# Performance work log

Hardware: AMD Instinct MI355X
Metric: run time of the kernel (lower is better)

The kernel has to match this reference:

```python
import jax, jax.numpy as jnp
import numpy as np

BN_EPS = 1e-5


def _bn_train(x, gamma, beta):
    # BatchNorm1d over channel dim (axis=1) of [B, C, L], training-mode batch stats
    m = jnp.mean(x, axis=(0, 2), keepdims=True)
    v = jnp.var(x, axis=(0, 2), keepdims=True)  # biased, matches torch normalization
    xn = (x - m) * jax.lax.rsqrt(v + BN_EPS)
    return xn * gamma[None, :, None] + beta[None, :, None]


def setup_inputs() -> dict:
    key = jax.random.key(0)
    ks = jax.random.split(key, 9)
    B, d1, d2, dout, p1, p2 = 16, 64, 64, 64, 256, 256
    ini1 = np.sqrt(3.0 / dout / d1)
    ini2 = np.sqrt(3.0 / dout / d2)
    u = lambda k, s, ini: jax.random.uniform(k, s, jnp.float32, -ini, ini)
    return {
        "A_AP": jax.random.normal(ks[0], (B, d1, p1), jnp.float32),
        "A_UE": jax.random.normal(ks[1], (B, d1, p2), jnp.float32),
        "H": jax.random.normal(ks[2], (B, d2, p1, p2), jnp.float32),
        "Q1_AP": u(ks[3], (dout, d1), ini1),
        "Q2_AP": u(ks[4], (dout, d1), ini1),
        "Q1_UE": u(ks[5], (dout, d1), ini1),
        "Q2_UE": u(ks[6], (dout, d1), ini1),
        "P1_AP": u(ks[7], (dout, d2), ini2),
        "P1_UE": u(ks[8], (dout, d2), ini2),
        "gamma": jnp.ones((dout,), jnp.float32),
        "beta": jnp.zeros((dout,), jnp.float32),
        "permutation_size1": p1,
        "permutation_size2": p2,
        "BATCH_SIZE": B,
    }


def reference(A_AP, A_UE, H, Q1_AP, Q2_AP, Q1_UE, Q2_UE, P1_AP, P1_UE,
              gamma, beta, permutation_size1, permutation_size2, BATCH_SIZE):
    # mean-aggregations
    ue_mean = jnp.mean(A_UE, axis=-1)          # [B, d1]
    ap_mean = jnp.mean(A_AP, axis=-1)          # [B, d1]
    h_mean_ue = jnp.mean(H, axis=-1)           # [B, d2, p1]
    h_mean_ap = jnp.mean(H, axis=-2)           # [B, d2, p2]

    ap1 = jnp.einsum('od,bdp->bop', Q1_AP, A_AP)                # [B, out, p1]
    ap2 = jnp.einsum('od,bd->bo', Q2_AP, ue_mean)[:, :, None]   # [B, out, 1]
    ap3 = jnp.einsum('od,bdp->bop', P1_AP, h_mean_ue)           # [B, out, p1]
    ue1 = jnp.einsum('od,bdp->bop', Q1_UE, A_UE)                # [B, out, p2]
    ue2 = jnp.einsum('od,bd->bo', Q2_UE, ap_mean)[:, :, None]   # [B, out, 1]
    ue3 = jnp.einsum('od,bdp->bop', P1_UE, h_mean_ap)           # [B, out, p2]

    out_ap = 2.0 * ap1 + 2.0 * ap2 + 0.1 * ap3
    out_ue = 2.0 * ue1 + 2.0 * ue2 + 0.1 * ue3
    out_ap = jax.nn.relu(out_ap)
    out_ue = jax.nn.relu(out_ue)
    out_ap = _bn_train(out_ap, gamma, beta)
    out_ue = _bn_train(out_ue, gamma, beta)
    return out_ap, out_ue
```

## Files before the change

kernel.cpp:

```cpp
#include <hip/hip_runtime.h>
#include <stdint.h>

#define WS_HMUE 0
#define WS_HMAP 262144
#define WS_APM  524288
#define WS_UEM  525312
#define WS_Z    526336

__global__ __launch_bounds__(256) void k_reduce(
    const float* __restrict__ H,
    const float* __restrict__ A_AP, const float* __restrict__ A_UE,
    float* __restrict__ ws)
{
    const int bid = blockIdx.x;
    const int tid = threadIdx.x;
    const int w = tid >> 6;
    const int lane = tid & 63;

    __shared__ float lds_row[256];
    __shared__ float lds_col[1024];

    if (bid < 1024) {
        const float4* Hs = (const float4*)(H + (size_t)bid * 65536);
        float c0 = 0.f, c1 = 0.f, c2 = 0.f, c3 = 0.f;

        #pragma unroll 8
        for (int it = 0; it < 64; ++it) {
            const int row = it * 4 + w;
            float4 v = Hs[row * 64 + lane];
            c0 += v.x; c1 += v.y; c2 += v.z; c3 += v.w;
            float rs = (v.x + v.y) + (v.z + v.w);
            rs += __shfl_xor(rs, 1);
            rs += __shfl_xor(rs, 2);
            rs += __shfl_xor(rs, 4);
            rs += __shfl_xor(rs, 8);
            rs += __shfl_xor(rs, 16);
            rs += __shfl_xor(rs, 32);
            if (lane == 0) lds_row[row] = rs;
        }
        ((float4*)lds_col)[w * 64 + lane] = make_float4(c0, c1, c2, c3);
        __syncthreads();
        const float cs = lds_col[tid] + lds_col[256 + tid]
                       + lds_col[512 + tid] + lds_col[768 + tid];
        const int oidx = bid * 256 + tid;
        ws[WS_HMAP + oidx] = cs * (1.f / 256.f);
        ws[WS_HMUE + oidx] = lds_row[tid] * (1.f / 256.f);
    } else {
        const int m = bid - 1024;
        const int r = m * 4 + w;
        const bool is_ap = (r < 1024);
        const float4* src = is_ap ? (const float4*)(A_AP + r * 256)
                                  : (const float4*)(A_UE + (r - 1024) * 256);
        float4 v = src[lane];
        float s = (v.x + v.y) + (v.z + v.w);
        s += __shfl_xor(s, 1);
        s += __shfl_xor(s, 2);
        s += __shfl_xor(s, 4);
        s += __shfl_xor(s, 8);
        s += __shfl_xor(s, 16);
        s += __shfl_xor(s, 32);
        if (lane == 0) {
            if (is_ap) ws[WS_APM + r] = s * (1.f / 256.f);
            else       ws[WS_UEM + (r - 1024)] = s * (1.f / 256.f);
        }
    }
}

__global__ __launch_bounds__(256) void k_z(
    const float* __restrict__ A_AP, const float* __restrict__ A_UE,
    const float* __restrict__ Q1_AP, const float* __restrict__ Q2_AP,
    const float* __restrict__ Q1_UE, const float* __restrict__ Q2_UE,
    const float* __restrict__ P1_AP, const float* __restrict__ P1_UE,
    const float* __restrict__ hmue, const float* __restrict__ hmap,
    const float* __restrict__ apm,  const float* __restrict__ uem,
    float* __restrict__ z)
{
    const int bid = blockIdx.x;
    const int g = bid >> 8;
    const int rem = bid & 255;
    const int b = rem >> 4;
    const int o0 = (rem & 15) * 4;
    const int p = threadIdx.x;

    const float* A  = g ? A_UE : A_AP;
    const float* hm = g ? hmap : hmue;
    const float* am = g ? apm  : uem;
    const float* Q1 = g ? Q1_UE : Q1_AP;
    const float* Q2 = g ? Q2_UE : Q2_AP;
    const float* P1 = g ? P1_UE : P1_AP;

    __shared__ float s2[4];
    if (threadIdx.x < 4) {
        const float* qr = Q2 + (o0 + threadIdx.x) * 64;
        const float* ar = am + b * 64;
        float s = 0.f;
        #pragma unroll
        for (int d = 0; d < 64; ++d) s += qr[d] * ar[d];
        s2[threadIdx.x] = s;
    }
    __syncthreads();

    float accQ[4] = {0.f, 0.f, 0.f, 0.f};
    float accP[4] = {0.f, 0.f, 0.f, 0.f};
    const float* Ab = A  + (b << 14) + p;
    const float* hb = hm + (b << 14) + p;

    #pragma unroll 4
    for (int dd = 0; dd < 16; ++dd) {
        const int d0 = dd * 4;
        float a0 = Ab[(d0 + 0) * 256];
        float a1 = Ab[(d0 + 1) * 256];
        float a2 = Ab[(d0 + 2) * 256];
        float a3 = Ab[(d0 + 3) * 256];
        float h0 = hb[(d0 + 0) * 256];
        float h1 = hb[(d0 + 1) * 256];
        float h2 = hb[(d0 + 2) * 256];
        float h3 = hb[(d0 + 3) * 256];
        #pragma unroll
        for (int j = 0; j < 4; ++j) {
            const float4 q  = *(const float4*)(Q1 + (o0 + j) * 64 + d0);
            const float4 pc = *(const float4*)(P1 + (o0 + j) * 64 + d0);
            accQ[j] += q.x * a0 + q.y * a1 + q.z * a2 + q.w * a3;
            accP[j] += pc.x * h0 + pc.y * h1 + pc.z * h2 + pc.w * h3;
        }
    }

    #pragma unroll
    for (int j = 0; j < 4; ++j) {
        float zv = 2.f * (accQ[j] + s2[j]) + 0.1f * accP[j];
        zv = fmaxf(zv, 0.f);
        z[((size_t)(g * 16 + b) * 64 + (o0 + j)) * 256 + p] = zv;
    }
}

__global__ __launch_bounds__(256) void k_bn(
    const float* __restrict__ z,
    const float* __restrict__ gamma, const float* __restrict__ beta,
    float* __restrict__ out)
{
    const int g = blockIdx.x >> 6;
    const int o = blockIdx.x & 63;
    const int t = threadIdx.x;
    const int w = t >> 6;
    const int lane = t & 63;

    const float* zp = z + (size_t)g * 262144 + o * 256 + t;
    float v[16];
    float s = 0.f, q = 0.f;
    #pragma unroll
    for (int b = 0; b < 16; ++b) {
        float x = zp[b * 16384];
        v[b] = x;
        s += x;
        q += x * x;
    }
    #pragma unroll
    for (int m = 1; m <= 32; m <<= 1) {
        s += __shfl_xor(s, m);
        q += __shfl_xor(q, m);
    }
    __shared__ float ls[4], lq[4];
    if (lane == 0) { ls[w] = s; lq[w] = q; }
    __syncthreads();
    s = ls[0] + ls[1] + ls[2] + ls[3];
    q = lq[0] + lq[1] + lq[2] + lq[3];

    const float mean = s * (1.f / 4096.f);
    const float var  = q * (1.f / 4096.f) - mean * mean;
    const float rstd = rsqrtf(var + 1e-5f);
    const float scale = rstd * gamma[o];
    const float shift = beta[o] - mean * scale;

    float* op = out + (size_t)g * 262144 + o * 256 + t;
    #pragma unroll
    for (int b = 0; b < 16; ++b)
        op[b * 16384] = v[b] * scale + shift;
}

extern "C" void kernel_launch(void* const* d_in, const int* in_sizes, int n_in,
                              void* d_out, int out_size, void* d_ws, size_t ws_size,
                              hipStream_t stream)
{
    const float* A_AP  = (const float*)d_in[0];
    const float* A_UE  = (const float*)d_in[1];
    const float* H     = (const float*)d_in[2];
    const float* Q1_AP = (const float*)d_in[3];
    const float* Q2_AP = (const float*)d_in[4];
    const float* Q1_UE = (const float*)d_in[5];
    const float* Q2_UE = (const float*)d_in[6];
    const float* P1_AP = (const float*)d_in[7];
    const float* P1_UE = (const float*)d_in[8];
    const float* gamma = (const float*)d_in[9];
    const float* beta  = (const float*)d_in[10];

    float* ws = (float*)d_ws;
    float* out = (float*)d_out;

    hipLaunchKernelGGL(k_reduce, dim3(1536), dim3(256), 0, stream,
                       H, A_AP, A_UE, ws);

    hipLaunchKernelGGL(k_z, dim3(512), dim3(256), 0, stream,
                       A_AP, A_UE, Q1_AP, Q2_AP, Q1_UE, Q2_UE, P1_AP, P1_UE,
                       ws + WS_HMUE, ws + WS_HMAP, ws + WS_APM, ws + WS_UEM,
                       ws + WS_Z);

    hipLaunchKernelGGL(k_bn, dim3(128), dim3(256), 0, stream,
                       ws + WS_Z, gamma, beta, out);
}
```

Baseline: 397.0 us.

## Fold A-mean reduction into H blocks, batch row shuffles, split k_z finer

The H reduction now loads four rows per iteration and merges their row sums with a transpose-style shuffle, which cuts the number of cross-lane shuffles per row. The separate A_AP/A_UE mean blocks are folded into the 1024 H blocks, handled by two waves each, so the grid drops to 1024 blocks. k_z now computes two output channels per block over 1024 blocks instead of four over 512, and its Q2 dot product becomes a wave-parallel shuffle reduction. This gives more parallelism in k_z, but each block re-reads the same A and H-mean rows, so redundant loads double.

```diff
diff --git a/kernel.cpp b/kernel.cpp
--- a/kernel.cpp
+++ b/kernel.cpp
@@ -12,47 +12,58 @@
     const float* __restrict__ A_AP, const float* __restrict__ A_UE,
     float* __restrict__ ws)
 {
-    const int bid = blockIdx.x;
-    const int tid = threadIdx.x;
-    const int w = tid >> 6;
+    const int bid  = blockIdx.x;
+    const int tid  = threadIdx.x;
+    const int w    = tid >> 6;
     const int lane = tid & 63;
 
     __shared__ float lds_row[256];
     __shared__ float lds_col[1024];
 
-    if (bid < 1024) {
-        const float4* Hs = (const float4*)(H + (size_t)bid * 65536);
-        float c0 = 0.f, c1 = 0.f, c2 = 0.f, c3 = 0.f;
-
-        #pragma unroll 8
-        for (int it = 0; it < 64; ++it) {
-            const int row = it * 4 + w;
-            float4 v = Hs[row * 64 + lane];
-            c0 += v.x; c1 += v.y; c2 += v.z; c3 += v.w;
-            float rs = (v.x + v.y) + (v.z + v.w);
-            rs += __shfl_xor(rs, 1);
-            rs += __shfl_xor(rs, 2);
-            rs += __shfl_xor(rs, 4);
-            rs += __shfl_xor(rs, 8);
-            rs += __shfl_xor(rs, 16);
-            rs += __shfl_xor(rs, 32);
-            if (lane == 0) lds_row[row] = rs;
-        }
-        ((float4*)lds_col)[w * 64 + lane] = make_float4(c0, c1, c2, c3);
-        __syncthreads();
-        const float cs = lds_col[tid] + lds_col[256 + tid]
-                       + lds_col[512 + tid] + lds_col[768 + tid];
-        const int oidx = bid * 256 + tid;
-        ws[WS_HMAP + oidx] = cs * (1.f / 256.f);
-        ws[WS_HMUE + oidx] = lds_row[tid] * (1.f / 256.f);
-    } else {
-        const int m = bid - 1024;
-        const int r = m * 4 + w;
+    const float4* Hs = (const float4*)(H + (size_t)bid * 65536);
+    float c0 = 0.f, c1 = 0.f, c2 = 0.f, c3 = 0.f;
+    const int b1 = lane & 1;
+    const int b2 = lane & 2;
+
+    #pragma unroll 2
+    for (int it = 0; it < 16; ++it) {
+        const int rbase = it * 16 + w * 4;
+        const float4 v0 = Hs[(rbase + 0) * 64 + lane];
+        const float4 v1 = Hs[(rbase + 1) * 64 + lane];
+        const float4 v2 = Hs[(rbase + 2) * 64 + lane];
+        const float4 v3 = Hs[(rbase + 3) * 64 + lane];
+        c0 += (v0.x + v1.x) + (v2.x + v3.x);
+        c1 += (v0.y + v1.y) + (v2.y + v3.y);
+        c2 += (v0.z + v1.z) + (v2.z + v3.z);
+        c3 += (v0.w + v1.w) + (v2.w + v3.w);
+        float rs0 = (v0.x + v0.y) + (v0.z + v0.w);
+        float rs1 = (v1.x + v1.y) + (v1.z + v1.w);
+        float rs2 = (v2.x + v2.y) + (v2.z + v2.w);
+        float rs3 = (v3.x + v3.y) + (v3.z + v3.w);
+        float s01 = (b1 ? rs1 : rs0) + __shfl_xor(b1 ? rs0 : rs1, 1);
+        float s23 = (b1 ? rs3 : rs2) + __shfl_xor(b1 ? rs2 : rs3, 1);
+        float s   = (b2 ? s23 : s01) + __shfl_xor(b2 ? s01 : s23, 2);
+        s += __shfl_xor(s, 4);
+        s += __shfl_xor(s, 8);
+        s += __shfl_xor(s, 16);
+        s += __shfl_xor(s, 32);
+        if (lane < 4) lds_row[rbase + lane] = s;
+    }
+    ((float4*)lds_col)[w * 64 + lane] = make_float4(c0, c1, c2, c3);
+    __syncthreads();
+    const float cs = lds_col[tid] + lds_col[256 + tid]
+                   + lds_col[512 + tid] + lds_col[768 + tid];
+    const int oidx = bid * 256 + tid;
+    ws[WS_HMAP + oidx] = cs * (1.f / 256.f);
+    ws[WS_HMUE + oidx] = lds_row[tid] * (1.f / 256.f);
+
+    if (w < 2) {
+        const int r = bid * 2 + w;
         const bool is_ap = (r < 1024);
-        const float4* src = is_ap ? (const float4*)(A_AP + r * 256)
-                                  : (const float4*)(A_UE + (r - 1024) * 256);
-        float4 v = src[lane];
-        float s = (v.x + v.y) + (v.z + v.w);
+        const float4* src = is_ap ? (const float4*)(A_AP + (size_t)r * 256)
+                                  : (const float4*)(A_UE + (size_t)(r - 1024) * 256);
+        const float4 vv = src[lane];
+        float s = (vv.x + vv.y) + (vv.z + vv.w);
         s += __shfl_xor(s, 1);
         s += __shfl_xor(s, 2);
         s += __shfl_xor(s, 4);
@@ -71,37 +82,40 @@
     const float* __restrict__ Q1_AP, const float* __restrict__ Q2_AP,
     const float* __restrict__ Q1_UE, const float* __restrict__ Q2_UE,
     const float* __restrict__ P1_AP, const float* __restrict__ P1_UE,
-    const float* __restrict__ hmue, const float* __restrict__ hmap,
-    const float* __restrict__ apm,  const float* __restrict__ uem,
-    float* __restrict__ z)
-{
+    const float* __restrict__ ws)
+{
+    float* wsm = (float*)ws;
     const int bid = blockIdx.x;
-    const int g = bid >> 8;
-    const int rem = bid & 255;
-    const int b = rem >> 4;
-    const int o0 = (rem & 15) * 4;
-    const int p = threadIdx.x;
+    const int g   = bid >> 9;
+    const int rem = bid & 511;
+    const int b   = rem >> 5;
+    const int o0  = (rem & 31) * 2;
+    const int p   = threadIdx.x;
+    const int w   = p >> 6;
+    const int lane = p & 63;
 
     const float* A  = g ? A_UE : A_AP;
-    const float* hm = g ? hmap : hmue;
-    const float* am = g ? apm  : uem;
+    const float* hm = ws + (g ? WS_HMAP : WS_HMUE);
+    const float* am = ws + (g ? WS_APM  : WS_UEM);
     const float* Q1 = g ? Q1_UE : Q1_AP;
     const float* Q2 = g ? Q2_UE : Q2_AP;
     const float* P1 = g ? P1_UE : P1_AP;
 
-    __shared__ float s2[4];
-    if (threadIdx.x < 4) {
-        const float* qr = Q2 + (o0 + threadIdx.x) * 64;
-        const float* ar = am + b * 64;
-        float s = 0.f;
-        #pragma unroll
-        for (int d = 0; d < 64; ++d) s += qr[d] * ar[d];
-        s2[threadIdx.x] = s;
+    __shared__ float s2[2];
+    if (w < 2) {
+        float pr = Q2[(o0 + w) * 64 + lane] * am[b * 64 + lane];
+        pr += __shfl_xor(pr, 1);
+        pr += __shfl_xor(pr, 2);
+        pr += __shfl_xor(pr, 4);
+        pr += __shfl_xor(pr, 8);
+        pr += __shfl_xor(pr, 16);
+        pr += __shfl_xor(pr, 32);
+        if (lane == 0) s2[w] = pr;
     }
     __syncthreads();
 
-    float accQ[4] = {0.f, 0.f, 0.f, 0.f};
-    float accP[4] = {0.f, 0.f, 0.f, 0.f};
+    float accQ[2] = {0.f, 0.f};
+    float accP[2] = {0.f, 0.f};
     const float* Ab = A  + (b << 14) + p;
     const float* hb = hm + (b << 14) + p;
 
@@ -117,7 +131,7 @@
         float h2 = hb[(d0 + 2) * 256];
         float h3 = hb[(d0 + 3) * 256];
         #pragma unroll
-        for (int j = 0; j < 4; ++j) {
+        for (int j = 0; j < 2; ++j) {
             const float4 q  = *(const float4*)(Q1 + (o0 + j) * 64 + d0);
             const float4 pc = *(const float4*)(P1 + (o0 + j) * 64 + d0);
             accQ[j] += q.x * a0 + q.y * a1 + q.z * a2 + q.w * a3;
@@ -126,10 +140,10 @@
     }
 
     #pragma unroll
-    for (int j = 0; j < 4; ++j) {
+    for (int j = 0; j < 2; ++j) {
         float zv = 2.f * (accQ[j] + s2[j]) + 0.1f * accP[j];
         zv = fmaxf(zv, 0.f);
-        z[((size_t)(g * 16 + b) * 64 + (o0 + j)) * 256 + p] = zv;
+        wsm[WS_Z + ((size_t)(g * 16 + b) * 64 + (o0 + j)) * 256 + p] = zv;
     }
 }
 
@@ -193,16 +207,15 @@
     const float* gamma = (const float*)d_in[9];
     const float* beta  = (const float*)d_in[10];
 
-    float* ws = (float*)d_ws;
+    float* ws  = (float*)d_ws;
     float* out = (float*)d_out;
 
-    hipLaunchKernelGGL(k_reduce, dim3(1536), dim3(256), 0, stream,
+    hipLaunchKernelGGL(k_reduce, dim3(1024), dim3(256), 0, stream,
                        H, A_AP, A_UE, ws);
 
-    hipLaunchKernelGGL(k_z, dim3(512), dim3(256), 0, stream,
+    hipLaunchKernelGGL(k_z, dim3(1024), dim3(256), 0, stream,
                        A_AP, A_UE, Q1_AP, Q2_AP, Q1_UE, Q2_UE, P1_AP, P1_UE,
-                       ws + WS_HMUE, ws + WS_HMAP, ws + WS_APM, ws + WS_UEM,
-                       ws + WS_Z);
+                       ws);
 
     hipLaunchKernelGGL(k_bn, dim3(128), dim3(256), 0, stream,
                        ws + WS_Z, gamma, beta, out);
```

After: 396.0 us. No clear change (-0.3%).
